# Performance work log

Hardware: AMD Instinct MI355X
Metric: run time of the kernel (lower is better)

Reference implementation:

```python
import jax, jax.numpy as jnp
import numpy as np

E = 19   # electrodes
H = 32   # lstm hidden dim per direction


def setup_inputs() -> dict:
    key = jax.random.key(0)
    ks = jax.random.split(key, 8)
    B, T = 64, 2048
    s = 1.0 / np.sqrt(H)  # PyTorch LSTM/Linear init scale
    u = lambda k, shp: jax.random.uniform(k, shp, jnp.float32, -s, s)
    return {
        "x": jax.random.normal(ks[0], (B, T, E), jnp.float32),
        # per-electrode, per-direction LSTM params (input_dim=1 so w_ih is a vector per gate block)
        "w_ih": u(ks[1], (E, 2, 4 * H)),          # [E, dir, 4H]
        "w_hh": u(ks[2], (E, 2, 4 * H, H)),       # [E, dir, 4H, H]
        "b_ih": u(ks[3], (E, 2, 4 * H)),
        "b_hh": u(ks[4], (E, 2, 4 * H)),
        "ln_gamma": jnp.ones((E, 2 * H), jnp.float32),
        "ln_beta": jnp.zeros((E, 2 * H), jnp.float32),
        "fc_w": u(ks[5], (1, 2 * H)),
        "fc_b": u(ks[6], (1,)),
    }


def reference(x, w_ih, w_hh, b_ih, b_hh, ln_gamma, ln_beta, fc_w, fc_b):
    B, T, E_ = x.shape
    # dir 0 = forward time, dir 1 = reversed time (bidirectional)
    xs = jnp.stack([x, x[:, ::-1, :]], axis=-1)      # [B, T, E, 2]
    xs = jnp.moveaxis(xs, 1, 0)                      # [T, B, E, 2]
    b = b_ih + b_hh                                  # [E, 2, 4H]

    h0 = jnp.zeros((B, E_, 2, H), x.dtype)
    c0 = jnp.zeros_like(h0)

    def step(carry, xt):
        h, c = carry
        # xt: [B, E, 2] scalar input per electrode/direction (input_dim == 1)
        gates = xt[..., None] * w_ih + jnp.einsum('bedh,edgh->bedg', h, w_hh) + b
        i, f, g, o = jnp.split(gates, 4, axis=-1)    # PyTorch gate order i,f,g,o
        c = jax.nn.sigmoid(f) * c + jax.nn.sigmoid(i) * jnp.tanh(g)
        h = jax.nn.sigmoid(o) * jnp.tanh(c)
        return (h, c), None

    (hT, _), _ = jax.lax.scan(step, (h0, c0), xs)
    # final hidden: dir0 = fwd at t=T-1 (hn[-2]), dir1 = bwd at t=0 (hn[-1]); concat features
    out = hT.reshape(B, E_, 2 * H)                   # [B, E, 64]

    # per-electrode LayerNorm over the 64-dim feature
    mu = out.mean(-1, keepdims=True)
    var = out.var(-1, keepdims=True)
    out = (out - mu) / jnp.sqrt(var + 1e-5) * ln_gamma + ln_beta

    pooled = out.mean(axis=1)                        # mean over electrodes -> [B, 64]
    logits = pooled @ fc_w.T + fc_b                  # [B, 1]
    return logits[:, 0]
```

## Files before the change

### kernel.cpp

```cpp
#include <hip/hip_runtime.h>
#include <math.h>
#include <stdint.h>

#define E_N 19
#define H_N 32
#define T_N 2048
#define B_N 64
#define G_N 128
#define XCHUNK 64
#define LOG2E 1.4426950408889634f

typedef _Float16 half2_t __attribute__((ext_vector_type(2)));

__device__ __forceinline__ float sigm_rcp(float e) {
    return __builtin_amdgcn_rcpf(1.0f + e);
}

__global__ __launch_bounds__(64)
__attribute__((amdgpu_waves_per_eu(3, 3)))
void lstm_chain_kernel(
    const float* __restrict__ x,
    const float* __restrict__ w_ih,
    const float* __restrict__ w_hh,
    const float* __restrict__ b_ih,
    const float* __restrict__ b_hh,
    float* __restrict__ hT)
{
    const int lane  = threadIdx.x;
    const int chain = blockIdx.x;
    const int b  = chain / (E_N * 2);
    const int ed = chain - b * (E_N * 2);
    const int e  = ed >> 1;
    const int d  = ed & 1;
    const int j    = lane & 31;
    const int half = lane >> 5;

    const int r1 = j + 32 * half;
    const int r2 = j + 64 + 32 * half;

    const float* wr1 = w_hh + ((size_t)ed * G_N + r1) * H_N;
    const float* wr2 = w_hh + ((size_t)ed * G_N + r2) * H_N;
    uint32_t w1p[16], w2p[16];
    #pragma unroll
    for (int m = 0; m < 16; ++m) {
        float2 v1 = ((const float2*)wr1)[m];
        float2 v2 = ((const float2*)wr2)[m];
        half2_t p1 = { (_Float16)v1.x, (_Float16)v1.y };
        half2_t p2 = { (_Float16)v2.x, (_Float16)v2.y };
        w1p[m] = __builtin_bit_cast(uint32_t, p1);
        w2p[m] = __builtin_bit_cast(uint32_t, p2);
    }

    const float wih1  = w_ih[(size_t)ed * G_N + r1];
    const float wih2  = w_ih[(size_t)ed * G_N + r2];
    const float bias1 = b_ih[(size_t)ed * G_N + r1] + b_hh[(size_t)ed * G_N + r1];
    const float bias2 = b_ih[(size_t)ed * G_N + r2] + b_hh[(size_t)ed * G_N + r2];

    const float K2 = half ? (-LOG2E) : (-2.0f * LOG2E);
    const float A2 = half ?  1.0f :  2.0f;
    const float B2 = half ?  0.0f : -1.0f;

    __shared__ __align__(16) uint16_t hbuf[64];
    __shared__ float xbuf[XCHUNK];

    if (lane < 32) hbuf[lane] = 0;
    float c = 0.0f;
    float h = 0.0f;

    const float* xbase = x + (size_t)b * T_N * E_N + e;
    const int hwr = j + 32 * (1 - half);

    for (int t0 = 0; t0 < T_N; t0 += XCHUNK) {
        #pragma unroll
        for (int m = 0; m < 16; ++m) {
            asm volatile("" : "+v"(w1p[m]), "+v"(w2p[m]));
        }

        const int tt    = t0 + lane;
        const int tphys = d ? (T_N - 1 - tt) : tt;
        xbuf[lane] = xbase[(size_t)tphys * E_N];

        #pragma unroll 1
        for (int tl = 0; tl < XCHUNK; ++tl) {
            const uint4 q0 = ((const uint4*)hbuf)[0];
            const uint4 q1 = ((const uint4*)hbuf)[1];
            const uint4 q2 = ((const uint4*)hbuf)[2];
            const uint4 q3 = ((const uint4*)hbuf)[3];
            const float sx = xbuf[tl];

            uint32_t hp[16];
            hp[0]=q0.x; hp[1]=q0.y; hp[2]=q0.z; hp[3]=q0.w;
            hp[4]=q1.x; hp[5]=q1.y; hp[6]=q1.z; hp[7]=q1.w;
            hp[8]=q2.x; hp[9]=q2.y; hp[10]=q2.z; hp[11]=q2.w;
            hp[12]=q3.x; hp[13]=q3.y; hp[14]=q3.z; hp[15]=q3.w;

            float a1 = fmaf(sx, wih1, bias1), a1b = 0.0f;
            float a2 = fmaf(sx, wih2, bias2), a2b = 0.0f;
            #pragma unroll
            for (int m = 0; m < 8; ++m) {
                a1  = __builtin_amdgcn_fdot2(__builtin_bit_cast(half2_t, hp[m]),
                                             __builtin_bit_cast(half2_t, w1p[m]),   a1,  false);
                a1b = __builtin_amdgcn_fdot2(__builtin_bit_cast(half2_t, hp[m+8]),
                                             __builtin_bit_cast(half2_t, w1p[m+8]), a1b, false);
                a2  = __builtin_amdgcn_fdot2(__builtin_bit_cast(half2_t, hp[m]),
                                             __builtin_bit_cast(half2_t, w2p[m]),   a2,  false);
                a2b = __builtin_amdgcn_fdot2(__builtin_bit_cast(half2_t, hp[m+8]),
                                             __builtin_bit_cast(half2_t, w2p[m+8]), a2b, false);
            }
            const float g1 = a1 + a1b;
            const float g2 = a2 + a2b;

            const float act1 = sigm_rcp(__builtin_amdgcn_exp2f(g1 * (-LOG2E)));
            const float act2 = fmaf(A2, sigm_rcp(__builtin_amdgcn_exp2f(g2 * K2)), B2);

            const float ig  = act1 * act2;
            const float igx = __shfl_xor(ig, 32);

            c = fmaf(act1, c, igx);
            const float tc = fmaf(2.0f, sigm_rcp(
                __builtin_amdgcn_exp2f(c * (-2.0f * LOG2E))), -1.0f);
            h = act2 * tc;

            hbuf[hwr] = __builtin_bit_cast(uint16_t, (_Float16)h);
        }
    }

    if (half) {
        hT[((size_t)(b * E_N + e) * 2 + d) * H_N + j] = h;
    }
}

__global__ __launch_bounds__(64) void head_kernel(
    const float* __restrict__ hT,
    const float* __restrict__ ln_gamma,
    const float* __restrict__ ln_beta,
    const float* __restrict__ fc_w,
    const float* __restrict__ fc_b,
    float* __restrict__ out)
{
    const int b = blockIdx.x;
    const int f = threadIdx.x;

    float acc = 0.0f;
    for (int e = 0; e < E_N; ++e) {
        const float v = hT[(size_t)(b * E_N + e) * 64 + f];
        float s = v, s2 = v * v;
        #pragma unroll
        for (int off = 32; off > 0; off >>= 1) {
            s  += __shfl_xor(s,  off);
            s2 += __shfl_xor(s2, off);
        }
        const float mean = s * (1.0f / 64.0f);
        const float var  = s2 * (1.0f / 64.0f) - mean * mean;
        const float inv  = rsqrtf(var + 1e-5f);
        acc += (v - mean) * inv * ln_gamma[e * 64 + f] + ln_beta[e * 64 + f];
    }
    float contrib = (acc * (1.0f / (float)E_N)) * fc_w[f];
    #pragma unroll
    for (int off = 32; off > 0; off >>= 1) contrib += __shfl_xor(contrib, off);
    if (f == 0) out[b] = contrib + fc_b[0];
}

extern "C" void kernel_launch(void* const* d_in, const int* in_sizes, int n_in,
                              void* d_out, int out_size, void* d_ws, size_t ws_size,
                              hipStream_t stream) {
    const float* x        = (const float*)d_in[0];
    const float* w_ih     = (const float*)d_in[1];
    const float* w_hh     = (const float*)d_in[2];
    const float* b_ih     = (const float*)d_in[3];
    const float* b_hh     = (const float*)d_in[4];
    const float* ln_gamma = (const float*)d_in[5];
    const float* ln_beta  = (const float*)d_in[6];
    const float* fc_w     = (const float*)d_in[7];
    const float* fc_b     = (const float*)d_in[8];
    float* out = (float*)d_out;
    float* hT  = (float*)d_ws;

    lstm_chain_kernel<<<B_N * E_N * 2, 64, 0, stream>>>(x, w_ih, w_hh, b_ih, b_hh, hT);
    head_kernel<<<B_N, 64, 0, stream>>>(hT, ln_gamma, ln_beta, fc_w, fc_b, out);
}
```

Measured before the change: 897.4 us.

## Pack two LSTM chains per wave with each lane computing all four gates

Each 64-lane block now runs two independent LSTM chains, one per half-wave. Each lane holds all four gate rows of W_hh in packed fp16 registers, so the cross-half shuffle is gone and the grid is halved. This doubles per-lane dot-product work and register use (occupancy hint lowered to 2 waves/EU, x chunk shrunk to 32) in exchange for using every lane on useful chains and removing the shuffle from the serial dependency chain.

```diff
diff --git a/kernel.cpp b/kernel.cpp
--- a/kernel.cpp
+++ b/kernel.cpp
@@ -7,7 +7,7 @@
 #define T_N 2048
 #define B_N 64
 #define G_N 128
-#define XCHUNK 64
+#define XCHUNK 32
 #define LOG2E 1.4426950408889634f
 
 typedef _Float16 half2_t __attribute__((ext_vector_type(2)));
@@ -17,7 +17,7 @@
 }
 
 __global__ __launch_bounds__(64)
-__attribute__((amdgpu_waves_per_eu(3, 3)))
+__attribute__((amdgpu_waves_per_eu(2, 2)))
 void lstm_chain_kernel(
     const float* __restrict__ x,
     const float* __restrict__ w_ih,
@@ -27,66 +27,58 @@
     float* __restrict__ hT)
 {
     const int lane  = threadIdx.x;
-    const int chain = blockIdx.x;
+    const int j     = lane & 31;
+    const int half  = lane >> 5;
+    const int chain = blockIdx.x * 2 + half;
     const int b  = chain / (E_N * 2);
     const int ed = chain - b * (E_N * 2);
     const int e  = ed >> 1;
     const int d  = ed & 1;
-    const int j    = lane & 31;
-    const int half = lane >> 5;
 
-    const int r1 = j + 32 * half;
-    const int r2 = j + 64 + 32 * half;
-
-    const float* wr1 = w_hh + ((size_t)ed * G_N + r1) * H_N;
-    const float* wr2 = w_hh + ((size_t)ed * G_N + r2) * H_N;
-    uint32_t w1p[16], w2p[16];
+    uint32_t wp[4][16];
+    float    wih[4], bias[4];
     #pragma unroll
-    for (int m = 0; m < 16; ++m) {
-        float2 v1 = ((const float2*)wr1)[m];
-        float2 v2 = ((const float2*)wr2)[m];
-        half2_t p1 = { (_Float16)v1.x, (_Float16)v1.y };
-        half2_t p2 = { (_Float16)v2.x, (_Float16)v2.y };
-        w1p[m] = __builtin_bit_cast(uint32_t, p1);
-        w2p[m] = __builtin_bit_cast(uint32_t, p2);
+    for (int gi = 0; gi < 4; ++gi) {
+        const int   row = j + 32 * gi;
+        const float* wr = w_hh + ((size_t)ed * G_N + row) * H_N;
+        #pragma unroll
+        for (int m = 0; m < 16; ++m) {
+            float2 v = ((const float2*)wr)[m];
+            half2_t p = { (_Float16)v.x, (_Float16)v.y };
+            wp[gi][m] = __builtin_bit_cast(uint32_t, p);
+        }
+        wih[gi]  = w_ih[(size_t)ed * G_N + row];
+        bias[gi] = b_ih[(size_t)ed * G_N + row] + b_hh[(size_t)ed * G_N + row];
     }
 
-    const float wih1  = w_ih[(size_t)ed * G_N + r1];
-    const float wih2  = w_ih[(size_t)ed * G_N + r2];
-    const float bias1 = b_ih[(size_t)ed * G_N + r1] + b_hh[(size_t)ed * G_N + r1];
-    const float bias2 = b_ih[(size_t)ed * G_N + r2] + b_hh[(size_t)ed * G_N + r2];
+    __shared__ __align__(16) uint16_t hbuf[2][H_N];
+    __shared__ float xbuf[2][XCHUNK];
 
-    const float K2 = half ? (-LOG2E) : (-2.0f * LOG2E);
-    const float A2 = half ?  1.0f :  2.0f;
-    const float B2 = half ?  0.0f : -1.0f;
-
-    __shared__ __align__(16) uint16_t hbuf[64];
-    __shared__ float xbuf[XCHUNK];
-
-    if (lane < 32) hbuf[lane] = 0;
+    hbuf[half][j] = 0;
     float c = 0.0f;
     float h = 0.0f;
 
     const float* xbase = x + (size_t)b * T_N * E_N + e;
-    const int hwr = j + 32 * (1 - half);
 
     for (int t0 = 0; t0 < T_N; t0 += XCHUNK) {
         #pragma unroll
         for (int m = 0; m < 16; ++m) {
-            asm volatile("" : "+v"(w1p[m]), "+v"(w2p[m]));
+            asm volatile("" : "+v"(wp[0][m]), "+v"(wp[1][m]),
+                              "+v"(wp[2][m]), "+v"(wp[3][m]));
         }
 
-        const int tt    = t0 + lane;
+        const int tt    = t0 + j;
         const int tphys = d ? (T_N - 1 - tt) : tt;
-        xbuf[lane] = xbase[(size_t)tphys * E_N];
+        xbuf[half][j] = xbase[(size_t)tphys * E_N];
 
         #pragma unroll 1
         for (int tl = 0; tl < XCHUNK; ++tl) {
-            const uint4 q0 = ((const uint4*)hbuf)[0];
-            const uint4 q1 = ((const uint4*)hbuf)[1];
-            const uint4 q2 = ((const uint4*)hbuf)[2];
-            const uint4 q3 = ((const uint4*)hbuf)[3];
-            const float sx = xbuf[tl];
+            const uint4* hb = (const uint4*)hbuf[half];
+            const uint4 q0 = hb[0];
+            const uint4 q1 = hb[1];
+            const uint4 q2 = hb[2];
+            const uint4 q3 = hb[3];
+            const float sx = xbuf[half][tl];
 
             uint32_t hp[16];
             hp[0]=q0.x; hp[1]=q0.y; hp[2]=q0.z; hp[3]=q0.w;
@@ -94,40 +86,45 @@
             hp[8]=q2.x; hp[9]=q2.y; hp[10]=q2.z; hp[11]=q2.w;
             hp[12]=q3.x; hp[13]=q3.y; hp[14]=q3.z; hp[15]=q3.w;
 
-            float a1 = fmaf(sx, wih1, bias1), a1b = 0.0f;
-            float a2 = fmaf(sx, wih2, bias2), a2b = 0.0f;
+            float ga[4], gb[4];
+            #pragma unroll
+            for (int gi = 0; gi < 4; ++gi) {
+                ga[gi] = fmaf(sx, wih[gi], bias[gi]);
+                gb[gi] = 0.0f;
+            }
             #pragma unroll
             for (int m = 0; m < 8; ++m) {
-                a1  = __builtin_amdgcn_fdot2(__builtin_bit_cast(half2_t, hp[m]),
-                                             __builtin_bit_cast(half2_t, w1p[m]),   a1,  false);
-                a1b = __builtin_amdgcn_fdot2(__builtin_bit_cast(half2_t, hp[m+8]),
-                                             __builtin_bit_cast(half2_t, w1p[m+8]), a1b, false);
-                a2  = __builtin_amdgcn_fdot2(__builtin_bit_cast(half2_t, hp[m]),
-                                             __builtin_bit_cast(half2_t, w2p[m]),   a2,  false);
-                a2b = __builtin_amdgcn_fdot2(__builtin_bit_cast(half2_t, hp[m+8]),
-                                             __builtin_bit_cast(half2_t, w2p[m+8]), a2b, false);
+                #pragma unroll
+                for (int gi = 0; gi < 4; ++gi) {
+                    ga[gi] = __builtin_amdgcn_fdot2(
+                        __builtin_bit_cast(half2_t, hp[m]),
+                        __builtin_bit_cast(half2_t, wp[gi][m]),   ga[gi], false);
+                    gb[gi] = __builtin_amdgcn_fdot2(
+                        __builtin_bit_cast(half2_t, hp[m+8]),
+                        __builtin_bit_cast(half2_t, wp[gi][m+8]), gb[gi], false);
+                }
             }
-            const float g1 = a1 + a1b;
-            const float g2 = a2 + a2b;
+            const float gi_v = ga[0] + gb[0];
+            const float gf_v = ga[1] + gb[1];
+            const float gg_v = ga[2] + gb[2];
+            const float go_v = ga[3] + gb[3];
 
-            const float act1 = sigm_rcp(__builtin_amdgcn_exp2f(g1 * (-LOG2E)));
-            const float act2 = fmaf(A2, sigm_rcp(__builtin_amdgcn_exp2f(g2 * K2)), B2);
+            const float si = sigm_rcp(__builtin_amdgcn_exp2f(gi_v * (-LOG2E)));
+            const float sf = sigm_rcp(__builtin_amdgcn_exp2f(gf_v * (-LOG2E)));
+            const float tg = fmaf(2.0f, sigm_rcp(
+                __builtin_amdgcn_exp2f(gg_v * (-2.0f * LOG2E))), -1.0f);
+            const float so = sigm_rcp(__builtin_amdgcn_exp2f(go_v * (-LOG2E)));
 
-            const float ig  = act1 * act2;
-            const float igx = __shfl_xor(ig, 32);
-
-            c = fmaf(act1, c, igx);
+            c = fmaf(sf, c, si * tg);
             const float tc = fmaf(2.0f, sigm_rcp(
                 __builtin_amdgcn_exp2f(c * (-2.0f * LOG2E))), -1.0f);
-            h = act2 * tc;
+            h = so * tc;
 
-            hbuf[hwr] = __builtin_bit_cast(uint16_t, (_Float16)h);
+            hbuf[half][j] = __builtin_bit_cast(uint16_t, (_Float16)h);
         }
     }
 
-    if (half) {
-        hT[((size_t)(b * E_N + e) * 2 + d) * H_N + j] = h;
-    }
+    hT[((size_t)(b * E_N + e) * 2 + d) * H_N + j] = h;
 }
 
 __global__ __launch_bounds__(64) void head_kernel(
@@ -176,6 +173,6 @@
     float* out = (float*)d_out;
     float* hT  = (float*)d_ws;
 
-    lstm_chain_kernel<<<B_N * E_N * 2, 64, 0, stream>>>(x, w_ih, w_hh, b_ih, b_hh, hT);
+    lstm_chain_kernel<<<(B_N * E_N * 2) / 2, 64, 0, stream>>>(x, w_ih, w_hh, b_ih, b_hh, hT);
     head_kernel<<<B_N, 64, 0, stream>>>(hT, ln_gamma, ln_beta, fc_w, fc_b, out);
 }
```

Result: slower. 973.1 us (+8.4%).

## Exchange LSTM hidden state via DPP pack and ds_bpermute instead of LDS

Applied to the files above, without the earlier changes.

Replaces the per-step LDS write/read of the fp16 hidden vector with a DPP lane swap, packed fp16 conversion, and 16 ds_bpermute broadcasts from the upper-half lanes. It also splits each gate dot product into four independent accumulation chains and applies the input term at the end to shorten the dependency chain. This trades four wide LDS loads plus a store for sixteen cross-lane permutes per timestep, which may or may not reduce serial latency.

```diff
diff --git a/kernel.cpp b/kernel.cpp
--- a/kernel.cpp
+++ b/kernel.cpp
@@ -11,9 +11,16 @@
 #define LOG2E 1.4426950408889634f
 
 typedef _Float16 half2_t __attribute__((ext_vector_type(2)));
+typedef __fp16   fp16v2  __attribute__((ext_vector_type(2)));
 
 __device__ __forceinline__ float sigm_rcp(float e) {
     return __builtin_amdgcn_rcpf(1.0f + e);
+}
+
+__device__ __forceinline__ uint32_t pack_h_pair(float h) {
+    const int hn = __builtin_amdgcn_mov_dpp(__float_as_int(h), 0xB1, 0xF, 0xF, false);
+    const fp16v2 pk = __builtin_amdgcn_cvt_pkrtz(h, __int_as_float(hn));
+    return __builtin_bit_cast(uint32_t, pk);
 }
 
 __global__ __launch_bounds__(64)
@@ -60,15 +67,13 @@
     const float A2 = half ?  1.0f :  2.0f;
     const float B2 = half ?  0.0f : -1.0f;
 
-    __shared__ __align__(16) uint16_t hbuf[64];
     __shared__ float xbuf[XCHUNK];
 
-    if (lane < 32) hbuf[lane] = 0;
     float c = 0.0f;
     float h = 0.0f;
+    uint32_t pk = 0u;
 
     const float* xbase = x + (size_t)b * T_N * E_N + e;
-    const int hwr = j + 32 * (1 - half);
 
     for (int t0 = 0; t0 < T_N; t0 += XCHUNK) {
         #pragma unroll
@@ -82,33 +87,36 @@
 
         #pragma unroll 1
         for (int tl = 0; tl < XCHUNK; ++tl) {
-            const uint4 q0 = ((const uint4*)hbuf)[0];
-            const uint4 q1 = ((const uint4*)hbuf)[1];
-            const uint4 q2 = ((const uint4*)hbuf)[2];
-            const uint4 q3 = ((const uint4*)hbuf)[3];
+            uint32_t hp[16];
+            #pragma unroll
+            for (int m = 0; m < 16; ++m) {
+                hp[m] = (uint32_t)__builtin_amdgcn_ds_bpermute(4 * (32 + 2 * m), (int)pk);
+            }
             const float sx = xbuf[tl];
 
-            uint32_t hp[16];
-            hp[0]=q0.x; hp[1]=q0.y; hp[2]=q0.z; hp[3]=q0.w;
-            hp[4]=q1.x; hp[5]=q1.y; hp[6]=q1.z; hp[7]=q1.w;
-            hp[8]=q2.x; hp[9]=q2.y; hp[10]=q2.z; hp[11]=q2.w;
-            hp[12]=q3.x; hp[13]=q3.y; hp[14]=q3.z; hp[15]=q3.w;
-
-            float a1 = fmaf(sx, wih1, bias1), a1b = 0.0f;
-            float a2 = fmaf(sx, wih2, bias2), a2b = 0.0f;
+            float s10 = bias1, s11 = 0.0f, s12 = 0.0f, s13 = 0.0f;
+            float s20 = bias2, s21 = 0.0f, s22 = 0.0f, s23 = 0.0f;
             #pragma unroll
-            for (int m = 0; m < 8; ++m) {
-                a1  = __builtin_amdgcn_fdot2(__builtin_bit_cast(half2_t, hp[m]),
-                                             __builtin_bit_cast(half2_t, w1p[m]),   a1,  false);
-                a1b = __builtin_amdgcn_fdot2(__builtin_bit_cast(half2_t, hp[m+8]),
-                                             __builtin_bit_cast(half2_t, w1p[m+8]), a1b, false);
-                a2  = __builtin_amdgcn_fdot2(__builtin_bit_cast(half2_t, hp[m]),
-                                             __builtin_bit_cast(half2_t, w2p[m]),   a2,  false);
-                a2b = __builtin_amdgcn_fdot2(__builtin_bit_cast(half2_t, hp[m+8]),
-                                             __builtin_bit_cast(half2_t, w2p[m+8]), a2b, false);
+            for (int m = 0; m < 4; ++m) {
+                s10 = __builtin_amdgcn_fdot2(__builtin_bit_cast(half2_t, hp[m]),
+                                             __builtin_bit_cast(half2_t, w1p[m]),    s10, false);
+                s11 = __builtin_amdgcn_fdot2(__builtin_bit_cast(half2_t, hp[m+4]),
+                                             __builtin_bit_cast(half2_t, w1p[m+4]),  s11, false);
+                s12 = __builtin_amdgcn_fdot2(__builtin_bit_cast(half2_t, hp[m+8]),
+                                             __builtin_bit_cast(half2_t, w1p[m+8]),  s12, false);
+                s13 = __builtin_amdgcn_fdot2(__builtin_bit_cast(half2_t, hp[m+12]),
+                                             __builtin_bit_cast(half2_t, w1p[m+12]), s13, false);
+                s20 = __builtin_amdgcn_fdot2(__builtin_bit_cast(half2_t, hp[m]),
+                                             __builtin_bit_cast(half2_t, w2p[m]),    s20, false);
+                s21 = __builtin_amdgcn_fdot2(__builtin_bit_cast(half2_t, hp[m+4]),
+                                             __builtin_bit_cast(half2_t, w2p[m+4]),  s21, false);
+                s22 = __builtin_amdgcn_fdot2(__builtin_bit_cast(half2_t, hp[m+8]),
+                                             __builtin_bit_cast(half2_t, w2p[m+8]),  s22, false);
+                s23 = __builtin_amdgcn_fdot2(__builtin_bit_cast(half2_t, hp[m+12]),
+                                             __builtin_bit_cast(half2_t, w2p[m+12]), s23, false);
             }
-            const float g1 = a1 + a1b;
-            const float g2 = a2 + a2b;
+            const float g1 = fmaf(sx, wih1, (s10 + s11) + (s12 + s13));
+            const float g2 = fmaf(sx, wih2, (s20 + s21) + (s22 + s23));
 
             const float act1 = sigm_rcp(__builtin_amdgcn_exp2f(g1 * (-LOG2E)));
             const float act2 = fmaf(A2, sigm_rcp(__builtin_amdgcn_exp2f(g2 * K2)), B2);
@@ -121,7 +129,7 @@
                 __builtin_amdgcn_exp2f(c * (-2.0f * LOG2E))), -1.0f);
             h = act2 * tc;
 
-            hbuf[hwr] = __builtin_bit_cast(uint16_t, (_Float16)h);
+            pk = pack_h_pair(h);
         }
     }
 
```

New measurement: 1.101 ms. 1.23x slower.

## Process two batch chains per wavefront sharing register-resident weights

Applied to the files above, without the earlier changes.

Each block now runs the LSTM recurrence for two batch elements of the same electrode/direction, reusing the fp16-packed recurrent weights held in registers. This halves the number of blocks and interleaves two independent dependency chains per wave for instruction-level parallelism. Occupancy hint lowered to 2 waves per EU to allow more registers. Risk: fewer waves may leave SIMDs underfilled or imbalanced, and the extra registers may cut latency hiding.

```diff
diff --git a/kernel.cpp b/kernel.cpp
--- a/kernel.cpp
+++ b/kernel.cpp
@@ -17,7 +17,7 @@
 }
 
 __global__ __launch_bounds__(64)
-__attribute__((amdgpu_waves_per_eu(3, 3)))
+__attribute__((amdgpu_waves_per_eu(2, 2)))
 void lstm_chain_kernel(
     const float* __restrict__ x,
     const float* __restrict__ w_ih,
@@ -26,12 +26,14 @@
     const float* __restrict__ b_hh,
     float* __restrict__ hT)
 {
-    const int lane  = threadIdx.x;
-    const int chain = blockIdx.x;
-    const int b  = chain / (E_N * 2);
-    const int ed = chain - b * (E_N * 2);
-    const int e  = ed >> 1;
-    const int d  = ed & 1;
+    const int lane = threadIdx.x;
+    const int pid  = blockIdx.x;
+    const int ed   = pid % (E_N * 2);
+    const int bp   = pid / (E_N * 2);
+    const int b0   = 2 * bp;
+    const int b1   = 2 * bp + 1;
+    const int e    = ed >> 1;
+    const int d    = ed & 1;
     const int j    = lane & 31;
     const int half = lane >> 5;
 
@@ -60,14 +62,16 @@
     const float A2 = half ?  1.0f :  2.0f;
     const float B2 = half ?  0.0f : -1.0f;
 
-    __shared__ __align__(16) uint16_t hbuf[64];
-    __shared__ float xbuf[XCHUNK];
-
-    if (lane < 32) hbuf[lane] = 0;
-    float c = 0.0f;
-    float h = 0.0f;
-
-    const float* xbase = x + (size_t)b * T_N * E_N + e;
+    __shared__ __align__(16) uint16_t hbuf[2][64];
+    __shared__ float xbuf[2][XCHUNK];
+
+    hbuf[0][lane] = 0;
+    hbuf[1][lane] = 0;
+    float c0 = 0.0f, h0 = 0.0f;
+    float c1 = 0.0f, h1 = 0.0f;
+
+    const float* xbase0 = x + (size_t)b0 * T_N * E_N + e;
+    const float* xbase1 = x + (size_t)b1 * T_N * E_N + e;
     const int hwr = j + 32 * (1 - half);
 
     for (int t0 = 0; t0 < T_N; t0 += XCHUNK) {
@@ -78,55 +82,83 @@
 
         const int tt    = t0 + lane;
         const int tphys = d ? (T_N - 1 - tt) : tt;
-        xbuf[lane] = xbase[(size_t)tphys * E_N];
+        xbuf[0][lane] = xbase0[(size_t)tphys * E_N];
+        xbuf[1][lane] = xbase1[(size_t)tphys * E_N];
 
         #pragma unroll 1
         for (int tl = 0; tl < XCHUNK; ++tl) {
-            const uint4 q0 = ((const uint4*)hbuf)[0];
-            const uint4 q1 = ((const uint4*)hbuf)[1];
-            const uint4 q2 = ((const uint4*)hbuf)[2];
-            const uint4 q3 = ((const uint4*)hbuf)[3];
-            const float sx = xbuf[tl];
-
-            uint32_t hp[16];
-            hp[0]=q0.x; hp[1]=q0.y; hp[2]=q0.z; hp[3]=q0.w;
-            hp[4]=q1.x; hp[5]=q1.y; hp[6]=q1.z; hp[7]=q1.w;
-            hp[8]=q2.x; hp[9]=q2.y; hp[10]=q2.z; hp[11]=q2.w;
-            hp[12]=q3.x; hp[13]=q3.y; hp[14]=q3.z; hp[15]=q3.w;
-
-            float a1 = fmaf(sx, wih1, bias1), a1b = 0.0f;
-            float a2 = fmaf(sx, wih2, bias2), a2b = 0.0f;
+            const uint4* hb0 = (const uint4*)hbuf[0];
+            const uint4* hb1 = (const uint4*)hbuf[1];
+            const uint4 a0 = hb0[0], a1 = hb0[1], a2 = hb0[2], a3 = hb0[3];
+            const uint4 d0 = hb1[0], d1 = hb1[1], d2 = hb1[2], d3 = hb1[3];
+            const float sx0 = xbuf[0][tl];
+            const float sx1 = xbuf[1][tl];
+
+            uint32_t hp0[16], hp1[16];
+            hp0[0]=a0.x; hp0[1]=a0.y; hp0[2]=a0.z; hp0[3]=a0.w;
+            hp0[4]=a1.x; hp0[5]=a1.y; hp0[6]=a1.z; hp0[7]=a1.w;
+            hp0[8]=a2.x; hp0[9]=a2.y; hp0[10]=a2.z; hp0[11]=a2.w;
+            hp0[12]=a3.x; hp0[13]=a3.y; hp0[14]=a3.z; hp0[15]=a3.w;
+            hp1[0]=d0.x; hp1[1]=d0.y; hp1[2]=d0.z; hp1[3]=d0.w;
+            hp1[4]=d1.x; hp1[5]=d1.y; hp1[6]=d1.z; hp1[7]=d1.w;
+            hp1[8]=d2.x; hp1[9]=d2.y; hp1[10]=d2.z; hp1[11]=d2.w;
+            hp1[12]=d3.x; hp1[13]=d3.y; hp1[14]=d3.z; hp1[15]=d3.w;
+
+            float s10 = fmaf(sx0, wih1, bias1), s11 = 0.0f;
+            float s20 = fmaf(sx0, wih2, bias2), s21 = 0.0f;
+            float u10 = fmaf(sx1, wih1, bias1), u11 = 0.0f;
+            float u20 = fmaf(sx1, wih2, bias2), u21 = 0.0f;
             #pragma unroll
             for (int m = 0; m < 8; ++m) {
-                a1  = __builtin_amdgcn_fdot2(__builtin_bit_cast(half2_t, hp[m]),
-                                             __builtin_bit_cast(half2_t, w1p[m]),   a1,  false);
-                a1b = __builtin_amdgcn_fdot2(__builtin_bit_cast(half2_t, hp[m+8]),
-                                             __builtin_bit_cast(half2_t, w1p[m+8]), a1b, false);
-                a2  = __builtin_amdgcn_fdot2(__builtin_bit_cast(half2_t, hp[m]),
-                                             __builtin_bit_cast(half2_t, w2p[m]),   a2,  false);
-                a2b = __builtin_amdgcn_fdot2(__builtin_bit_cast(half2_t, hp[m+8]),
-                                             __builtin_bit_cast(half2_t, w2p[m+8]), a2b, false);
+                s10 = __builtin_amdgcn_fdot2(__builtin_bit_cast(half2_t, hp0[m]),
+                                             __builtin_bit_cast(half2_t, w1p[m]),   s10, false);
+                s11 = __builtin_amdgcn_fdot2(__builtin_bit_cast(half2_t, hp0[m+8]),
+                                             __builtin_bit_cast(half2_t, w1p[m+8]), s11, false);
+                s20 = __builtin_amdgcn_fdot2(__builtin_bit_cast(half2_t, hp0[m]),
+                                             __builtin_bit_cast(half2_t, w2p[m]),   s20, false);
+                s21 = __builtin_amdgcn_fdot2(__builtin_bit_cast(half2_t, hp0[m+8]),
+                                             __builtin_bit_cast(half2_t, w2p[m+8]), s21, false);
+                u10 = __builtin_amdgcn_fdot2(__builtin_bit_cast(half2_t, hp1[m]),
+                                             __builtin_bit_cast(half2_t, w1p[m]),   u10, false);
+                u11 = __builtin_amdgcn_fdot2(__builtin_bit_cast(half2_t, hp1[m+8]),
+                                             __builtin_bit_cast(half2_t, w1p[m+8]), u11, false);
+                u20 = __builtin_amdgcn_fdot2(__builtin_bit_cast(half2_t, hp1[m]),
+                                             __builtin_bit_cast(half2_t, w2p[m]),   u20, false);
+                u21 = __builtin_amdgcn_fdot2(__builtin_bit_cast(half2_t, hp1[m+8]),
+                                             __builtin_bit_cast(half2_t, w2p[m+8]), u21, false);
             }
-            const float g1 = a1 + a1b;
-            const float g2 = a2 + a2b;
-
-            const float act1 = sigm_rcp(__builtin_amdgcn_exp2f(g1 * (-LOG2E)));
-            const float act2 = fmaf(A2, sigm_rcp(__builtin_amdgcn_exp2f(g2 * K2)), B2);
-
-            const float ig  = act1 * act2;
-            const float igx = __shfl_xor(ig, 32);
-
-            c = fmaf(act1, c, igx);
-            const float tc = fmaf(2.0f, sigm_rcp(
-                __builtin_amdgcn_exp2f(c * (-2.0f * LOG2E))), -1.0f);
-            h = act2 * tc;
-
-            hbuf[hwr] = __builtin_bit_cast(uint16_t, (_Float16)h);
+            const float g1_0 = s10 + s11;
+            const float g2_0 = s20 + s21;
+            const float g1_1 = u10 + u11;
+            const float g2_1 = u20 + u21;
+
+            const float act1_0 = sigm_rcp(__builtin_amdgcn_exp2f(g1_0 * (-LOG2E)));
+            const float act2_0 = fmaf(A2, sigm_rcp(__builtin_amdgcn_exp2f(g2_0 * K2)), B2);
+            const float act1_1 = sigm_rcp(__builtin_amdgcn_exp2f(g1_1 * (-LOG2E)));
+            const float act2_1 = fmaf(A2, sigm_rcp(__builtin_amdgcn_exp2f(g2_1 * K2)), B2);
+
+            const float ig0  = act1_0 * act2_0;
+            const float ig1  = act1_1 * act2_1;
+            const float igx0 = __shfl_xor(ig0, 32);
+            const float igx1 = __shfl_xor(ig1, 32);
+
+            c0 = fmaf(act1_0, c0, igx0);
+            c1 = fmaf(act1_1, c1, igx1);
+            const float tc0 = fmaf(2.0f, sigm_rcp(
+                __builtin_amdgcn_exp2f(c0 * (-2.0f * LOG2E))), -1.0f);
+            const float tc1 = fmaf(2.0f, sigm_rcp(
+                __builtin_amdgcn_exp2f(c1 * (-2.0f * LOG2E))), -1.0f);
+            h0 = act2_0 * tc0;
+            h1 = act2_1 * tc1;
+
+            hbuf[0][hwr] = __builtin_bit_cast(uint16_t, (_Float16)h0);
+            hbuf[1][hwr] = __builtin_bit_cast(uint16_t, (_Float16)h1);
         }
     }
 
     if (half) {
-        hT[((size_t)(b * E_N + e) * 2 + d) * H_N + j] = h;
+        hT[((size_t)(b0 * E_N + e) * 2 + d) * H_N + j] = h0;
+        hT[((size_t)(b1 * E_N + e) * 2 + d) * H_N + j] = h1;
     }
 }
 
@@ -176,6 +208,6 @@
     float* out = (float*)d_out;
     float* hT  = (float*)d_ws;
 
-    lstm_chain_kernel<<<B_N * E_N * 2, 64, 0, stream>>>(x, w_ih, w_hh, b_ih, b_hh, hT);
+    lstm_chain_kernel<<<(B_N / 2) * E_N * 2, 64, 0, stream>>>(x, w_ih, w_hh, b_ih, b_hh, hT);
     head_kernel<<<B_N, 64, 0, stream>>>(hT, ln_gamma, ln_beta, fc_w, fc_b, out);
 }
```

Measured after the change: 1.104 ms. 1.23x slower.
